# Kernel tuning notes

Measured on AMD Instinct MI355X. Metric: run time of the kernel, lower is better.

Reference implementation:

```python
import jax, jax.numpy as jnp
import numpy as np
from jax import lax

B, T, P, I, H = 1024, 100, 50, 96, 1024  # batch, seq_dim, pred_dim, input_dim, hidden_dim


def _gru_cell(x, h, Wih, Whh, bih, bhh):
    # PyTorch GRU gate math. Wih:[3H,in], Whh:[3H,H]
    gi = x @ Wih.T + bih
    gh = h @ Whh.T + bhh
    ir, iz, i_n = jnp.split(gi, 3, axis=-1)
    hr, hz, h_n = jnp.split(gh, 3, axis=-1)
    r = jax.nn.sigmoid(ir + hr)
    z = jax.nn.sigmoid(iz + hz)
    n = jnp.tanh(i_n + r * h_n)
    return (1.0 - z) * n + z * h


def setup_inputs() -> dict:
    key = jax.random.key(0)
    ks = jax.random.split(key, 24)
    s = 1.0 / np.sqrt(H)

    def rn(k, shape):
        return jax.random.normal(k, shape, jnp.float32) * s

    inp = {"x": jax.random.normal(ks[0], (B, T, I), jnp.float32)}
    # encoder nn.GRU: layer 0 input I, layer 1 input H
    inp["enc_Wih0"] = rn(ks[1], (3 * H, I)); inp["enc_Whh0"] = rn(ks[2], (3 * H, H))
    inp["enc_bih0"] = rn(ks[3], (3 * H,));   inp["enc_bhh0"] = rn(ks[4], (3 * H,))
    inp["enc_Wih1"] = rn(ks[5], (3 * H, H)); inp["enc_Whh1"] = rn(ks[6], (3 * H, H))
    inp["enc_bih1"] = rn(ks[7], (3 * H,));   inp["enc_bhh1"] = rn(ks[8], (3 * H,))
    # decoder GRUCells (hidden->hidden)
    inp["dec_Wih0"] = rn(ks[9], (3 * H, H)); inp["dec_Whh0"] = rn(ks[10], (3 * H, H))
    inp["dec_bih0"] = rn(ks[11], (3 * H,));  inp["dec_bhh0"] = rn(ks[12], (3 * H,))
    inp["dec_Wih1"] = rn(ks[13], (3 * H, H)); inp["dec_Whh1"] = rn(ks[14], (3 * H, H))
    inp["dec_bih1"] = rn(ks[15], (3 * H,));  inp["dec_bhh1"] = rn(ks[16], (3 * H,))
    # fc_in: I->H, fc_out: H->I
    inp["fc_in_w"] = rn(ks[17], (H, I)); inp["fc_in_b"] = rn(ks[18], (H,))
    inp["fc_out_w"] = rn(ks[19], (I, H)); inp["fc_out_b"] = rn(ks[20], (I,))
    return inp


def reference(x, enc_Wih0, enc_Whh0, enc_bih0, enc_bhh0,
              enc_Wih1, enc_Whh1, enc_bih1, enc_bhh1,
              dec_Wih0, dec_Whh0, dec_bih0, dec_bhh0,
              dec_Wih1, dec_Whh1, dec_bih1, dec_bhh1,
              fc_in_w, fc_in_b, fc_out_w, fc_out_b):
    b = x.shape[0]
    h0 = jnp.zeros((b, H), x.dtype)
    xs = jnp.transpose(x[:, :P, :], (1, 0, 2))  # [P, B, I]

    def enc0(h, xt):
        h2 = _gru_cell(xt, h, enc_Wih0, enc_Whh0, enc_bih0, enc_bhh0)
        return h2, h2

    h_enc0, seq0 = lax.scan(enc0, h0, xs)

    def enc1(h, xt):
        h2 = _gru_cell(xt, h, enc_Wih1, enc_Whh1, enc_bih1, enc_bhh1)
        return h2, h2

    h_enc1, _ = lax.scan(enc1, h0, seq0)

    def dec_step(carry, _):
        frame, hd0, hd1 = carry
        y = frame @ fc_in_w.T + fc_in_b
        hd0 = _gru_cell(y, hd0, dec_Wih0, dec_Whh0, dec_bih0, dec_bhh0)
        hd1 = _gru_cell(hd0, hd1, dec_Wih1, dec_Whh1, dec_bih1, dec_bhh1)
        frame = hd1 @ fc_out_w.T + fc_out_b + frame
        return (frame, hd0, hd1), frame

    init = (x[:, P - 1, :], h_enc0, h_enc1)
    _, outs = lax.scan(dec_step, init, None, length=T - P)  # [T-P, B, I]
    out = jnp.concatenate([x[:, :P, :], jnp.transpose(outs, (1, 0, 2))], axis=1)
    return out
```

## Files before the change

### kernel.cpp

```cpp
#include <hip/hip_runtime.h>
#include <hip/hip_bf16.h>
#include <stdint.h>

#define Bsz 1024
#define Tt  100
#define Pp  50
#define Ii  96
#define Hh  1024
#define H3  3072

typedef __bf16 bf16x8 __attribute__((ext_vector_type(8)));
typedef float f32x4 __attribute__((ext_vector_type(4)));
typedef __hip_bfloat16 bf16;

__device__ __forceinline__ void llds16(const void* g, void* l) {
    __builtin_amdgcn_global_load_lds(
        (const __attribute__((address_space(1))) void*)g,
        (__attribute__((address_space(3))) void*)l,
        16, 0, 0);
}

__device__ __forceinline__ f32x4 ldb4(const bf16* p) {
    ushort4 u = *(const ushort4*)p;
    union { unsigned int i; float f; } c;
    f32x4 r;
    c.i = (unsigned int)u.x << 16; r[0] = c.f;
    c.i = (unsigned int)u.y << 16; r[1] = c.f;
    c.i = (unsigned int)u.z << 16; r[2] = c.f;
    c.i = (unsigned int)u.w << 16; r[3] = c.f;
    return r;
}

__device__ __forceinline__ void swz_decomp(int& bx, int& by, int& bz) {
    int gx = gridDim.x, gy = gridDim.y, gz = gridDim.z;
    int flat = blockIdx.x + gx * (blockIdx.y + gy * blockIdx.z);
    int tot = gx * gy * gz;
    if (!(tot & 7)) {
        int q = tot >> 3;
        flat = (flat & 7) * q + (flat >> 3);
    }
    bx = flat % gx;
    int rest = flat / gx;
    by = rest % gy;
    bz = rest / gy;
}

__global__ void wdesc_k(unsigned long long* slot, const void* A, const void* W,
                        const void* b, void* C, int K, int lda) {
    if (threadIdx.x == 0) {
        slot[0] = (unsigned long long)A;
        slot[1] = (unsigned long long)W;
        slot[2] = (unsigned long long)b;
        slot[3] = (unsigned long long)C;
        slot[4] = (unsigned long long)K;
        slot[5] = (unsigned long long)lda;
    }
}

__global__ void __launch_bounds__(256)
gemm_tab(const unsigned long long* __restrict__ tab, int base, int ndesc,
         const bf16* __restrict__ extraA)
{
    __shared__ bf16 As[128 * 64];
    __shared__ bf16 Ws[128 * 64];
    int flat = blockIdx.x;
    const int tot = ndesc * 192;
    if (!(tot & 7)) {
        int q = tot >> 3;
        flat = (flat & 7) * q + (flat >> 3);
    }
    const int g = flat / 192;
    const int local = flat - g * 192;
    const unsigned long long* dp = tab + (size_t)(base + g) * 8;
    const bf16* A = (const bf16*)dp[0];
    const bf16* W = (const bf16*)dp[1];
    const float* bias = (const float*)dp[2];
    bf16* C = (bf16*)dp[3];
    const int K = (int)dp[4];
    const int lda = (int)dp[5];
    if (!A) A = extraA;

    const int tn = (local % 24) * 128;
    const int tm = (local / 24) * 128;

    const int tid = threadIdx.x;
    const int lane = tid & 63;
    const int wid = tid >> 6;
    const int wr = (wid >> 1) * 64;
    const int wc = (wid & 1) * 64;
    const int srow = tid >> 3;
    const int schk = ((tid & 7) ^ (srow & 7)) * 8;
    const int sdst = tid * 16;
    const int fr = lane & 15;
    const int hi = lane >> 4;

    f32x4 acc[4][4] = {};

    const bf16* ga = A + (size_t)(tm + srow) * lda + schk;
    const bf16* gw = W + (size_t)(tn + srow) * K + schk;
    char* lA = (char*)As + sdst;
    char* lW = (char*)Ws + sdst;
    const int nk = K >> 6;

    for (int kt = 0; kt < nk; ++kt) {
#pragma unroll
        for (int m = 0; m < 4; ++m) {
            llds16(ga + (size_t)(32 * m) * lda, lA + 32 * m * 128);
            llds16(gw + (size_t)(32 * m) * K,  lW + 32 * m * 128);
        }
        ga += 64; gw += 64;
        __syncthreads();

#pragma unroll
        for (int kk = 0; kk < 2; ++kk) {
            bf16x8 af[4], wf[4];
            const int chk = (((kk << 2) + hi) ^ (fr & 7)) * 8;
#pragma unroll
            for (int i = 0; i < 4; ++i) {
                af[i] = *(const bf16x8*)&As[(wr + i * 16 + fr) * 64 + chk];
                wf[i] = *(const bf16x8*)&Ws[(wc + i * 16 + fr) * 64 + chk];
            }
#pragma unroll
            for (int mi = 0; mi < 4; ++mi)
#pragma unroll
                for (int ni = 0; ni < 4; ++ni)
                    acc[mi][ni] = __builtin_amdgcn_mfma_f32_16x16x32_bf16(
                        af[mi], wf[ni], acc[mi][ni], 0, 0, 0);
        }
        __syncthreads();
    }

    const int fq = hi * 4;
#pragma unroll
    for (int mi = 0; mi < 4; ++mi)
#pragma unroll
        for (int ni = 0; ni < 4; ++ni) {
            const int col = tn + wc + ni * 16 + fr;
            const float bv = bias[col];
#pragma unroll
            for (int r = 0; r < 4; ++r) {
                const int row = tm + wr + mi * 16 + fq + r;
                C[(size_t)row * H3 + col] = __float2bfloat16(acc[mi][ni][r] + bv);
            }
        }
}

__global__ void __launch_bounds__(256)
fuse_fg_k(const float* __restrict__ gp,
          const float* __restrict__ fin,
          float* __restrict__ fout,
          float* __restrict__ out_t,
          const bf16* __restrict__ W,
          const float* __restrict__ bias,
          bf16* __restrict__ C)
{
    __shared__ bf16 Af[128 * 136];
    __shared__ bf16 Ws[128 * 64];
    int flat = blockIdx.x;
    { int q = 192 >> 3; flat = (flat & 7) * q + (flat >> 3); }
    const int tn = (flat % 24) * 128;
    const int tm = (flat / 24) * 128;
    const int tid = threadIdx.x;

#pragma unroll
    for (int i = 0; i < 12; ++i) {
        int v = i * 256 + tid;
        int row = v / 24;
        int c4 = (v % 24) * 4;
        size_t go = (size_t)(tm + row) * Ii + c4;
        f32x4 s = {};
#pragma unroll
        for (int p = 0; p < 8; ++p)
            s += *(const f32x4*)(gp + (size_t)p * (Bsz * Ii) + go);
        f32x4 fv = *(const f32x4*)(fin + go) + s;
        if (tn == 0) {
            *(f32x4*)(fout + go) = fv;
            *(f32x4*)(out_t + (size_t)(tm + row) * (Tt * Ii) + c4) = fv;
        }
        ushort4 up;
        unsigned short* us = &up.x;
#pragma unroll
        for (int e = 0; e < 4; ++e) {
            bf16 bv = __float2bfloat16(fv[e]);
            us[e] = *(unsigned short*)&bv;
        }
        *(ushort4*)&Af[row * 136 + c4] = up;
    }
#pragma unroll
    for (int i = 0; i < 4; ++i) {
        int v = i * 256 + tid;
        int row = v >> 3;
        int c4 = 96 + (v & 7) * 4;
        ushort4 z; z.x = 0; z.y = 0; z.z = 0; z.w = 0;
        *(ushort4*)&Af[row * 136 + c4] = z;
    }

    const int lane = tid & 63;
    const int wid = tid >> 6;
    const int wr = (wid >> 1) * 64;
    const int wc = (wid & 1) * 64;
    const int srow = tid >> 3;
    const int schk = ((tid & 7) ^ (srow & 7)) * 8;
    const int sdst = tid * 16;
    const int fr = lane & 15;
    const int hi = lane >> 4;

    f32x4 acc[4][4] = {};
    const bf16* gw = W + (size_t)(tn + srow) * 128 + schk;
    char* lW = (char*)Ws + sdst;

    for (int kt = 0; kt < 2; ++kt) {
#pragma unroll
        for (int m = 0; m < 4; ++m)
            llds16(gw + (size_t)(32 * m) * 128, lW + 32 * m * 128);
        gw += 64;
        __syncthreads();
#pragma unroll
        for (int kk = 0; kk < 2; ++kk) {
            bf16x8 af[4], wf[4];
            const int wchk = (((kk << 2) + hi) ^ (fr & 7)) * 8;
            const int achk = kt * 64 + ((kk << 2) + hi) * 8;
#pragma unroll
            for (int i = 0; i < 4; ++i) {
                af[i] = *(const bf16x8*)&Af[(wr + i * 16 + fr) * 136 + achk];
                wf[i] = *(const bf16x8*)&Ws[(wc + i * 16 + fr) * 64 + wchk];
            }
#pragma unroll
            for (int mi = 0; mi < 4; ++mi)
#pragma unroll
                for (int ni = 0; ni < 4; ++ni)
                    acc[mi][ni] = __builtin_amdgcn_mfma_f32_16x16x32_bf16(
                        af[mi], wf[ni], acc[mi][ni], 0, 0, 0);
        }
        __syncthreads();
    }

    const int fq = hi * 4;
#pragma unroll
    for (int mi = 0; mi < 4; ++mi)
#pragma unroll
        for (int ni = 0; ni < 4; ++ni) {
            const int col = tn + wc + ni * 16 + fr;
            const float bv = bias[col];
#pragma unroll
            for (int r = 0; r < 4; ++r) {
                const int row = tm + wr + mi * 16 + fq + r;
                C[(size_t)row * H3 + col] = __float2bfloat16(acc[mi][ni][r] + bv);
            }
        }
}

template <bool OUT_BF16>
__global__ void __launch_bounds__(256)
gemm64(const bf16* __restrict__ A, const bf16* __restrict__ W,
       const float* __restrict__ bias, void* __restrict__ Cout,
       int M, int Nreal, int Ktot, int Ks, int lda, int ldc)
{
    __shared__ bf16 As[64 * 32];
    __shared__ bf16 Ws[64 * 32];
    int bx, by, bz;
    swz_decomp(bx, by, bz);
    const int s = bz;
    const float* bs = (s == 0) ? bias : nullptr;
    const int tid = threadIdx.x;
    const int lane = tid & 63;
    const int wid = tid >> 6;
    const int wr = (wid >> 1) * 32;
    const int wc = (wid & 1) * 32;
    const int tm = by * 64;
    const int tn = bx * 64;
    const int srow = tid >> 2;
    const int skb = (tid & 3) * 8;
    const int k0 = s * Ks;

    f32x4 acc[2][2] = {};

    const bf16* ga = A + (size_t)(tm + srow) * lda + k0 + skb;
    const bf16* gw = W + (size_t)(tn + srow) * Ktot + k0 + skb;
    bf16* lA = &As[srow * 32 + skb];
    bf16* lW = &Ws[srow * 32 + skb];
    const int nk = Ks >> 5;

    for (int kt = 0; kt < nk; ++kt) {
        llds16(ga, lA);
        llds16(gw, lW);
        ga += 32; gw += 32;
        __syncthreads();
        const int fr = lane & 15;
        const int kg = (lane >> 4) * 8;
        bf16x8 af[2], wf[2];
#pragma unroll
        for (int i = 0; i < 2; ++i) {
            af[i] = *(const bf16x8*)&As[(wr + i * 16 + fr) * 32 + kg];
            wf[i] = *(const bf16x8*)&Ws[(wc + i * 16 + fr) * 32 + kg];
        }
#pragma unroll
        for (int mi = 0; mi < 2; ++mi)
#pragma unroll
            for (int ni = 0; ni < 2; ++ni)
                acc[mi][ni] = __builtin_amdgcn_mfma_f32_16x16x32_bf16(
                    af[mi], wf[ni], acc[mi][ni], 0, 0, 0);
        __syncthreads();
    }

    float* Cf = (float*)Cout + (size_t)s * M * ldc;
    const int fr = lane & 15;
    const int fq = (lane >> 4) * 4;
#pragma unroll
    for (int mi = 0; mi < 2; ++mi)
#pragma unroll
        for (int ni = 0; ni < 2; ++ni) {
            const int col = tn + wc + ni * 16 + fr;
            if (col < Nreal) {
                const float bv = bs ? bs[col] : 0.f;
#pragma unroll
                for (int r = 0; r < 4; ++r) {
                    const int row = tm + wr + mi * 16 + fq + r;
                    const float v = acc[mi][ni][r] + bv;
                    if constexpr (OUT_BF16)
                        ((bf16*)Cout)[(size_t)row * ldc + col] = __float2bfloat16(v);
                    else
                        Cf[(size_t)row * ldc + col] = v;
                }
            }
        }
}

__global__ void cvt_k(const float* __restrict__ s, bf16* __restrict__ d, int n) {
    int i = blockIdx.x * blockDim.x + threadIdx.x;
    if (i < n) d[i] = __float2bfloat16(s[i]);
}

__global__ void cvtpad_k(const float* __restrict__ s, bf16* __restrict__ d, int n) {
    int o = blockIdx.x * blockDim.x + threadIdx.x;
    if (o >= n * 128) return;
    int r = o >> 7, c = o & 127;
    d[o] = __float2bfloat16(c < Ii ? s[(size_t)r * Ii + c] : 0.f);
}

__global__ void tpose_k(const float* __restrict__ x, bf16* __restrict__ d) {
    int o = blockIdx.x * blockDim.x + threadIdx.x;
    if (o >= Tt * Bsz * 128) return;
    int i = o & 127;
    int b = (o >> 7) & (Bsz - 1);
    int t = o >> 17;
    d[o] = __float2bfloat16(i < Ii ? x[((size_t)b * Tt + t) * Ii + i] : 0.f);
}

__global__ void tposeFcin_k(const float* __restrict__ w, bf16* __restrict__ d) {
    int o = blockIdx.x * blockDim.x + threadIdx.x;
    if (o >= 128 * Hh) return;
    int r = o >> 10;
    int c = o & (Hh - 1);
    float v = (r < Ii) ? w[(size_t)c * Ii + r] : 0.f;
    d[o] = __float2bfloat16(v);
}

__global__ void __launch_bounds__(256)
bcomb_k(const float* __restrict__ W, const float* __restrict__ v,
        const float* __restrict__ b2, float* __restrict__ o) {
    __shared__ float red[256];
    int n = blockIdx.x;
    float s = 0.f;
    for (int k = threadIdx.x; k < Hh; k += 256)
        s += W[(size_t)n * Hh + k] * v[k];
    red[threadIdx.x] = s;
    __syncthreads();
    for (int w = 128; w > 0; w >>= 1) {
        if (threadIdx.x < w) red[threadIdx.x] += red[threadIdx.x + w];
        __syncthreads();
    }
    if (threadIdx.x == 0) o[n] = red[0] + b2[n];
}

__global__ void prefix_k(const float* __restrict__ x, float* __restrict__ out) {
    int idx = blockIdx.x * blockDim.x + threadIdx.x;
    if (idx >= Bsz * Pp * Ii) return;
    int b = idx / (Pp * Ii);
    int r = idx % (Pp * Ii);
    out[(size_t)b * Tt * Ii + r] = x[(size_t)b * Tt * Ii + r];
}

__global__ void finit_k(const float* __restrict__ x, float* __restrict__ fr,
                        bf16* __restrict__ frb) {
    int idx = blockIdx.x * blockDim.x + threadIdx.x;
    if (idx >= Bsz * Ii) return;
    int b = idx / Ii;
    int i = idx % Ii;
    float v = x[(size_t)b * Tt * Ii + (Pp - 1) * Ii + i];
    fr[idx] = v;
    frb[(size_t)b * 128 + i] = __float2bfloat16(v);
}

#define CELL_BODY(IDX, GI, GH, H, HB)                                        \
    {                                                                        \
        int b_ = (IDX) >> 8;                                                 \
        int j_ = ((IDX) & 255) << 2;                                         \
        size_t base_ = (size_t)b_ * H3 + j_;                                 \
        f32x4 ir = ldb4((GI) + base_);                                       \
        f32x4 iz = ldb4((GI) + base_ + Hh);                                  \
        f32x4 in = ldb4((GI) + base_ + 2 * Hh);                              \
        f32x4 hr = ldb4((GH) + base_);                                       \
        f32x4 hz = ldb4((GH) + base_ + Hh);                                  \
        f32x4 hn = ldb4((GH) + base_ + 2 * Hh);                              \
        size_t hoff_ = (size_t)b_ * Hh + j_;                                 \
        f32x4 hold = *(const f32x4*)((H) + hoff_);                           \
        f32x4 hv;                                                            \
        ushort4 up;                                                          \
        unsigned short* us = &up.x;                                          \
        _Pragma("unroll")                                                    \
        for (int e = 0; e < 4; ++e) {                                        \
            float r = 1.f / (1.f + __expf(-(ir[e] + hr[e])));                \
            float z = 1.f / (1.f + __expf(-(iz[e] + hz[e])));                \
            float n = tanhf(in[e] + r * hn[e]);                              \
            float v = (1.f - z) * n + z * hold[e];                           \
            hv[e] = v;                                                       \
            bf16 bv = __float2bfloat16(v);                                   \
            us[e] = *(unsigned short*)&bv;                                   \
        }                                                                    \
        *(f32x4*)((H) + hoff_) = hv;                                         \
        *(ushort4*)((unsigned short*)(HB) + hoff_) = up;                     \
    }

__global__ void __launch_bounds__(256)
gru_cell_k(const bf16* __restrict__ gi, const bf16* __restrict__ gh,
           float* __restrict__ h, bf16* __restrict__ hb) {
    int idx = blockIdx.x * 256 + threadIdx.x;
    CELL_BODY(idx, gi, gh, h, hb);
}

__global__ void __launch_bounds__(256)
gru_cell2_k(const bf16* __restrict__ giA, const bf16* __restrict__ ghA,
            float* __restrict__ hA, bf16* __restrict__ hbA,
            const bf16* __restrict__ giB, const bf16* __restrict__ ghB,
            float* __restrict__ hB, bf16* __restrict__ hbB) {
    int bid = blockIdx.x;
    const bf16* gi = giA;
    const bf16* gh = ghA;
    float* h = hA;
    bf16* hb = hbA;
    if (bid >= 1024) {
        gi = giB; gh = ghB; h = hB; hb = hbB;
        bid -= 1024;
    }
    int idx = bid * 256 + threadIdx.x;
    CELL_BODY(idx, gi, gh, h, hb);
}

extern "C" void kernel_launch(void* const* d_in, const int* in_sizes, int n_in,
                              void* d_out, int out_size, void* d_ws, size_t ws_size,
                              hipStream_t stream) {
    const float* x      = (const float*)d_in[0];
    const float* eWih0  = (const float*)d_in[1];
    const float* eWhh0  = (const float*)d_in[2];
    const float* ebih0  = (const float*)d_in[3];
    const float* ebhh0  = (const float*)d_in[4];
    const float* eWih1  = (const float*)d_in[5];
    const float* eWhh1  = (const float*)d_in[6];
    const float* ebih1  = (const float*)d_in[7];
    const float* ebhh1  = (const float*)d_in[8];
    const float* dWih0  = (const float*)d_in[9];
    const float* dWhh0  = (const float*)d_in[10];
    const float* dbih0  = (const float*)d_in[11];
    const float* dbhh0  = (const float*)d_in[12];
    const float* dWih1  = (const float*)d_in[13];
    const float* dWhh1  = (const float*)d_in[14];
    const float* dbih1  = (const float*)d_in[15];
    const float* dbhh1  = (const float*)d_in[16];
    const float* fcin_w = (const float*)d_in[17];
    const float* fcin_b = (const float*)d_in[18];
    const float* fcout_w= (const float*)d_in[19];
    const float* fcout_b= (const float*)d_in[20];
    float* out = (float*)d_out;

    char* base = (char*)d_ws;
    size_t off = 0;
    auto alloc = [&](size_t bytes) -> void* {
        void* r = base + off;
        off += (bytes + 255) & ~(size_t)255;
        return r;
    };
    bf16* wWih0e = (bf16*)alloc((size_t)H3 * 128 * 2);
    bf16* wWhh0e = (bf16*)alloc((size_t)H3 * Hh * 2);
    bf16* wWih1e = (bf16*)alloc((size_t)H3 * Hh * 2);
    bf16* wWhh1e = (bf16*)alloc((size_t)H3 * Hh * 2);
    bf16* wWhh0d = (bf16*)alloc((size_t)H3 * Hh * 2);
    bf16* wWih1d = (bf16*)alloc((size_t)H3 * Hh * 2);
    bf16* wWhh1d = (bf16*)alloc((size_t)H3 * Hh * 2);
    bf16* wWih0d = (bf16*)alloc((size_t)H3 * Hh * 2);
    bf16* fcinT  = (bf16*)alloc((size_t)128 * Hh * 2);
    bf16* wWcomb = (bf16*)alloc((size_t)H3 * 128 * 2);
    float* bcomb = (float*)alloc((size_t)H3 * 4);
    bf16* wfcout = (bf16*)alloc((size_t)128 * Hh * 2);
    float* zbias = (float*)alloc((size_t)128 * 4);
    bf16* xbT    = (bf16*)alloc((size_t)Tt * Bsz * 128 * 2);
    bf16* gi1_p  = (bf16*)alloc((size_t)Bsz * H3 * 2);
    bf16* gh1_p  = (bf16*)alloc((size_t)Bsz * H3 * 2);
    bf16* gh0_p  = (bf16*)alloc((size_t)Bsz * H3 * 2);
    bf16* gi0_p  = (bf16*)alloc((size_t)Bsz * H3 * 2);
    float* h0    = (float*)alloc((size_t)Bsz * Hh * 4);
    float* h1    = (float*)alloc((size_t)Bsz * Hh * 4);
    bf16* h0b    = (bf16*)alloc((size_t)Bsz * Hh * 2);
    bf16* h1b    = (bf16*)alloc((size_t)Bsz * Hh * 2);
    float* gfc   = (float*)alloc((size_t)8 * Bsz * Ii * 4);
    float* fbuf0 = (float*)alloc((size_t)Bsz * Ii * 4);
    float* fbuf1 = (float*)alloc((size_t)Bsz * Ii * 4);
    bf16* frameb = (bf16*)alloc((size_t)Bsz * 128 * 2);
    unsigned long long* tab = (unsigned long long*)alloc(8 * 8 * 8);
    if (off > ws_size) return;

    auto cvt = [&](const float* s, bf16* d, int n) {
        cvt_k<<<dim3((n + 255) / 256), dim3(256), 0, stream>>>(s, d, n);
    };
    cvtpad_k<<<dim3((H3 * 128 + 255) / 256), dim3(256), 0, stream>>>(eWih0, wWih0e, H3);
    cvt(eWhh0, wWhh0e, H3 * Hh);
    cvt(eWih1, wWih1e, H3 * Hh);
    cvt(eWhh1, wWhh1e, H3 * Hh);
    cvt(dWih0, wWih0d, H3 * Hh);
    cvt(dWhh0, wWhh0d, H3 * Hh);
    cvt(dWih1, wWih1d, H3 * Hh);
    cvt(dWhh1, wWhh1d, H3 * Hh);
    (void)hipMemsetAsync(wfcout, 0, (size_t)128 * Hh * 2, stream);
    (void)hipMemsetAsync(wWcomb, 0, (size_t)H3 * 128 * 2, stream);
    (void)hipMemsetAsync(zbias, 0, (size_t)128 * 4, stream);
    (void)hipMemsetAsync(frameb, 0, (size_t)Bsz * 128 * 2, stream);
    cvt(fcout_w, wfcout, Ii * Hh);
    tposeFcin_k<<<dim3((128 * Hh + 255) / 256), dim3(256), 0, stream>>>(fcin_w, fcinT);
    gemm64<true><<<dim3(2, 48, 1), dim3(256), 0, stream>>>(
        wWih0d, fcinT, zbias, (void*)wWcomb, H3, Ii, Hh, Hh, Hh, 128);
    bcomb_k<<<dim3(H3), dim3(256), 0, stream>>>(dWih0, fcin_b, dbih0, bcomb);

    tpose_k<<<dim3((Tt * Bsz * 128 + 255) / 256), dim3(256), 0, stream>>>(x, xbT);
    prefix_k<<<dim3((Bsz * Pp * Ii + 255) / 256), dim3(256), 0, stream>>>(x, out);
    finit_k<<<dim3((Bsz * Ii + 255) / 256), dim3(256), 0, stream>>>(x, fbuf0, frameb);
    (void)hipMemsetAsync(h0, 0, (size_t)Bsz * Hh * 4, stream);
    (void)hipMemsetAsync(h1, 0, (size_t)Bsz * Hh * 4, stream);
    (void)hipMemsetAsync(h0b, 0, (size_t)Bsz * Hh * 2, stream);
    (void)hipMemsetAsync(h1b, 0, (size_t)Bsz * Hh * 2, stream);

    wdesc_k<<<1, 64, 0, stream>>>(tab + 0 * 8, h0b, wWih1e, ebih1, gi1_p, Hh, Hh);
    wdesc_k<<<1, 64, 0, stream>>>(tab + 1 * 8, h1b, wWhh1e, ebhh1, gh1_p, Hh, Hh);
    wdesc_k<<<1, 64, 0, stream>>>(tab + 2 * 8, h0b, wWhh0e, ebhh0, gh0_p, Hh, Hh);
    wdesc_k<<<1, 64, 0, stream>>>(tab + 3 * 8, nullptr, wWih0e, ebih0, gi0_p, 128, 128);
    wdesc_k<<<1, 64, 0, stream>>>(tab + 4 * 8, h0b, wWih1d, dbih1, gi1_p, Hh, Hh);
    wdesc_k<<<1, 64, 0, stream>>>(tab + 5 * 8, h1b, wWhh1d, dbhh1, gh1_p, Hh, Hh);
    wdesc_k<<<1, 64, 0, stream>>>(tab + 6 * 8, h0b, wWhh0d, dbhh0, gh0_p, Hh, Hh);
    wdesc_k<<<1, 64, 0, stream>>>(tab + 7 * 8, frameb, wWcomb, bcomb, gi0_p, 128, 128);

    gemm_tab<<<dim3(384), dim3(256), 0, stream>>>(tab, 2, 2, xbT);
    gru_cell_k<<<dim3(1024), dim3(256), 0, stream>>>(gi0_p, gh0_p, h0, h0b);
    for (int i = 0; i < Pp; ++i) {
        if (i < Pp - 1) {
            gemm_tab<<<dim3(768), dim3(256), 0, stream>>>(
                tab, 0, 4, xbT + (size_t)(i + 1) * Bsz * 128);
            gru_cell2_k<<<dim3(2048), dim3(256), 0, stream>>>(
                gi1_p, gh1_p, h1, h1b, gi0_p, gh0_p, h0, h0b);
        } else {
            gemm_tab<<<dim3(384), dim3(256), 0, stream>>>(tab, 0, 2, xbT);
            gru_cell_k<<<dim3(1024), dim3(256), 0, stream>>>(gi1_p, gh1_p, h1, h1b);
        }
    }

    gemm_tab<<<dim3(384), dim3(256), 0, stream>>>(tab, 6, 2, xbT);
    gru_cell_k<<<dim3(1024), dim3(256), 0, stream>>>(gi0_p, gh0_p, h0, h0b);
    for (int t = 0; t < Tt - Pp; ++t) {
        const bool last = (t == Tt - Pp - 1);
        if (!last) {
            gemm_tab<<<dim3(576), dim3(256), 0, stream>>>(tab, 4, 3, xbT);
        } else {
            gemm_tab<<<dim3(384), dim3(256), 0, stream>>>(tab, 4, 2, xbT);
        }
        gru_cell_k<<<dim3(1024), dim3(256), 0, stream>>>(gi1_p, gh1_p, h1, h1b);
        gemm64<false><<<dim3(2, 16, 8), dim3(256), 0, stream>>>(
            h1b, wfcout, fcout_b, (void*)gfc, Bsz, Ii, Hh, Hh / 8, Hh, Ii);
        fuse_fg_k<<<dim3(192), dim3(256), 0, stream>>>(
            gfc, (t & 1) ? fbuf1 : fbuf0, (t & 1) ? fbuf0 : fbuf1,
            out + (size_t)(Pp + t) * Ii, wWcomb, bcomb, gi0_p);
        if (!last) {
            gru_cell_k<<<dim3(1024), dim3(256), 0, stream>>>(gi0_p, gh0_p, h0, h0b);
        }
    }
}
```

Baseline: 5.073 ms.

## Fuse decoder GRU cells into fc_out and gi0 GEMM kernels

In the decoder loop the layer-1 GRU cell is merged with the split-K fc_out GEMM (cellfc_k), and the gi0 GEMM is merged with the layer-0 GRU cell epilogue (megafuse_k). This cuts per-step launches from five to three and skips the round trips of gi0 and separate cell passes through global memory. Layer-1 hidden state is now double-buffered so cellfc_k's split-K blocks can read the old h1 while others write the new one. The fused kernels run on fewer blocks (256 and 128), which lowers parallelism. The last step now also runs the layer-0 cell update, which is wasted work.

```diff
diff --git a/kernel.cpp b/kernel.cpp
--- a/kernel.cpp
+++ b/kernel.cpp
@@ -29,6 +29,12 @@
     c.i = (unsigned int)u.z << 16; r[2] = c.f;
     c.i = (unsigned int)u.w << 16; r[3] = c.f;
     return r;
+}
+
+__device__ __forceinline__ float b2f(bf16 v) {
+    union { unsigned int i; float f; } c;
+    c.i = (unsigned int)(*(unsigned short*)&v) << 16;
+    return c.f;
 }
 
 __device__ __forceinline__ void swz_decomp(int& bx, int& by, int& bz) {
@@ -146,24 +152,130 @@
 }
 
 __global__ void __launch_bounds__(256)
-fuse_fg_k(const float* __restrict__ gp,
-          const float* __restrict__ fin,
-          float* __restrict__ fout,
-          float* __restrict__ out_t,
-          const bf16* __restrict__ W,
-          const float* __restrict__ bias,
-          bf16* __restrict__ C)
+cellfc_k(const bf16* __restrict__ gi, const bf16* __restrict__ gh,
+         const float* __restrict__ hin, float* __restrict__ hout,
+         bf16* __restrict__ hb,
+         const bf16* __restrict__ W,
+         const float* __restrict__ bias,
+         float* __restrict__ gfc)
 {
-    __shared__ bf16 Af[128 * 136];
+    __shared__ bf16 Af[64 * 136];
+    __shared__ bf16 Ws[64 * 32];
+    int flat = blockIdx.x;
+    { int q = 256 >> 3; flat = (flat & 7) * q + (flat >> 3); }
+    const int s = flat >> 5;
+    const int rest = flat & 31;
+    const int tm = (rest >> 1) * 64;
+    const int tn = (rest & 1) * 64;
+    const int k0 = s * 128;
+    const int tid = threadIdx.x;
+
+#pragma unroll
+    for (int i = 0; i < 8; ++i) {
+        int c = i * 256 + tid;
+        int row = c >> 5;
+        int c4 = (c & 31) * 4;
+        int b = tm + row;
+        int j = k0 + c4;
+        size_t gbase = (size_t)b * H3 + j;
+        f32x4 ir = ldb4(gi + gbase);
+        f32x4 iz = ldb4(gi + gbase + Hh);
+        f32x4 in = ldb4(gi + gbase + 2 * Hh);
+        f32x4 hr = ldb4(gh + gbase);
+        f32x4 hz = ldb4(gh + gbase + Hh);
+        f32x4 hn = ldb4(gh + gbase + 2 * Hh);
+        size_t ho = (size_t)b * Hh + j;
+        f32x4 hold = *(const f32x4*)(hin + ho);
+        f32x4 hv;
+        ushort4 up;
+        unsigned short* us = &up.x;
+#pragma unroll
+        for (int e = 0; e < 4; ++e) {
+            float r = 1.f / (1.f + __expf(-(ir[e] + hr[e])));
+            float z = 1.f / (1.f + __expf(-(iz[e] + hz[e])));
+            float n = tanhf(in[e] + r * hn[e]);
+            float v = (1.f - z) * n + z * hold[e];
+            hv[e] = v;
+            bf16 bv = __float2bfloat16(v);
+            us[e] = *(unsigned short*)&bv;
+        }
+        *(f32x4*)(hout + ho) = hv;
+        *(ushort4*)((unsigned short*)hb + ho) = up;
+        *(ushort4*)&Af[row * 136 + c4] = up;
+    }
+    __syncthreads();
+
+    const int lane = tid & 63;
+    const int wid = tid >> 6;
+    const int wr = (wid >> 1) * 32;
+    const int wc = (wid & 1) * 32;
+    const int srow = tid >> 2;
+    const int skb = (tid & 3) * 8;
+    const int fr = lane & 15;
+    const int kg = (lane >> 4) * 8;
+
+    f32x4 acc[2][2] = {};
+    const bf16* gw = W + (size_t)(tn + srow) * Hh + k0 + skb;
+    bf16* lW = &Ws[srow * 32 + skb];
+
+    for (int kt = 0; kt < 4; ++kt) {
+        llds16(gw, lW);
+        gw += 32;
+        __syncthreads();
+        bf16x8 af[2], wf[2];
+#pragma unroll
+        for (int i = 0; i < 2; ++i) {
+            af[i] = *(const bf16x8*)&Af[(wr + i * 16 + fr) * 136 + kt * 32 + kg];
+            wf[i] = *(const bf16x8*)&Ws[(wc + i * 16 + fr) * 32 + kg];
+        }
+#pragma unroll
+        for (int mi = 0; mi < 2; ++mi)
+#pragma unroll
+            for (int ni = 0; ni < 2; ++ni)
+                acc[mi][ni] = __builtin_amdgcn_mfma_f32_16x16x32_bf16(
+                    af[mi], wf[ni], acc[mi][ni], 0, 0, 0);
+        __syncthreads();
+    }
+
+    float* Cf = gfc + (size_t)s * (Bsz * Ii);
+    const int fq = (lane >> 4) * 4;
+#pragma unroll
+    for (int mi = 0; mi < 2; ++mi)
+#pragma unroll
+        for (int ni = 0; ni < 2; ++ni) {
+            const int col = tn + wc + ni * 16 + fr;
+            if (col < Ii) {
+                const float bv = (s == 0) ? bias[col] : 0.f;
+#pragma unroll
+                for (int r = 0; r < 4; ++r) {
+                    const int row = tm + wr + mi * 16 + fq + r;
+                    Cf[(size_t)row * Ii + col] = acc[mi][ni][r] + bv;
+                }
+            }
+        }
+}
+
+__global__ void __launch_bounds__(256)
+megafuse_k(const float* __restrict__ gp,
+           const float* __restrict__ fin,
+           float* __restrict__ fout,
+           float* __restrict__ out_t,
+           const bf16* __restrict__ W,
+           const float* __restrict__ bias,
+           const bf16* __restrict__ gh,
+           float* __restrict__ h,
+           bf16* __restrict__ hb)
+{
+    __shared__ bf16 Af[64 * 136];
     __shared__ bf16 Ws[128 * 64];
     int flat = blockIdx.x;
-    { int q = 192 >> 3; flat = (flat & 7) * q + (flat >> 3); }
-    const int tn = (flat % 24) * 128;
-    const int tm = (flat / 24) * 128;
+    { int q = 128 >> 3; flat = (flat & 7) * q + (flat >> 3); }
+    const int tm = (flat >> 3) * 64;
+    const int jt = flat & 7;
     const int tid = threadIdx.x;
 
 #pragma unroll
-    for (int i = 0; i < 12; ++i) {
+    for (int i = 0; i < 6; ++i) {
         int v = i * 256 + tid;
         int row = v / 24;
         int c4 = (v % 24) * 4;
@@ -173,7 +285,7 @@
         for (int p = 0; p < 8; ++p)
             s += *(const f32x4*)(gp + (size_t)p * (Bsz * Ii) + go);
         f32x4 fv = *(const f32x4*)(fin + go) + s;
-        if (tn == 0) {
+        if (jt == 0) {
             *(f32x4*)(fout + go) = fv;
             *(f32x4*)(out_t + (size_t)(tm + row) * (Tt * Ii) + c4) = fv;
         }
@@ -187,7 +299,7 @@
         *(ushort4*)&Af[row * 136 + c4] = up;
     }
 #pragma unroll
-    for (int i = 0; i < 4; ++i) {
+    for (int i = 0; i < 2; ++i) {
         int v = i * 256 + tid;
         int row = v >> 3;
         int c4 = 96 + (v & 7) * 4;
@@ -197,55 +309,74 @@
 
     const int lane = tid & 63;
     const int wid = tid >> 6;
-    const int wr = (wid >> 1) * 64;
+    const int wr = (wid >> 1) * 32;
     const int wc = (wid & 1) * 64;
     const int srow = tid >> 3;
     const int schk = ((tid & 7) ^ (srow & 7)) * 8;
     const int sdst = tid * 16;
     const int fr = lane & 15;
     const int hi = lane >> 4;
-
-    f32x4 acc[4][4] = {};
-    const bf16* gw = W + (size_t)(tn + srow) * 128 + schk;
     char* lW = (char*)Ws + sdst;
 
-    for (int kt = 0; kt < 2; ++kt) {
-#pragma unroll
-        for (int m = 0; m < 4; ++m)
-            llds16(gw + (size_t)(32 * m) * 128, lW + 32 * m * 128);
-        gw += 64;
-        __syncthreads();
-#pragma unroll
-        for (int kk = 0; kk < 2; ++kk) {
-            bf16x8 af[4], wf[4];
-            const int wchk = (((kk << 2) + hi) ^ (fr & 7)) * 8;
-            const int achk = kt * 64 + ((kk << 2) + hi) * 8;
-#pragma unroll
-            for (int i = 0; i < 4; ++i) {
-                af[i] = *(const bf16x8*)&Af[(wr + i * 16 + fr) * 136 + achk];
-                wf[i] = *(const bf16x8*)&Ws[(wc + i * 16 + fr) * 64 + wchk];
+    f32x4 acc[3][2][4] = {};
+#pragma unroll
+    for (int g = 0; g < 3; ++g) {
+        const bf16* gw = W + (size_t)(g * 1024 + jt * 128 + srow) * 128 + schk;
+        for (int kt = 0; kt < 2; ++kt) {
+            __syncthreads();
+#pragma unroll
+            for (int m = 0; m < 4; ++m)
+                llds16(gw + (size_t)(32 * m) * 128, lW + 32 * m * 128);
+            gw += 64;
+            __syncthreads();
+#pragma unroll
+            for (int kk = 0; kk < 2; ++kk) {
+                bf16x8 af[2], wf[4];
+                const int wchk = (((kk << 2) + hi) ^ (fr & 7)) * 8;
+                const int achk = kt * 64 + ((kk << 2) + hi) * 8;
+#pragma unroll
+                for (int i = 0; i < 2; ++i)
+                    af[i] = *(const bf16x8*)&Af[(wr + i * 16 + fr) * 136 + achk];
+#pragma unroll
+                for (int i = 0; i < 4; ++i)
+                    wf[i] = *(const bf16x8*)&Ws[(wc + i * 16 + fr) * 64 + wchk];
+#pragma unroll
+                for (int mi = 0; mi < 2; ++mi)
+#pragma unroll
+                    for (int ni = 0; ni < 4; ++ni)
+                        acc[g][mi][ni] = __builtin_amdgcn_mfma_f32_16x16x32_bf16(
+                            af[mi], wf[ni], acc[g][mi][ni], 0, 0, 0);
             }
-#pragma unroll
-            for (int mi = 0; mi < 4; ++mi)
-#pragma unroll
-                for (int ni = 0; ni < 4; ++ni)
-                    acc[mi][ni] = __builtin_amdgcn_mfma_f32_16x16x32_bf16(
-                        af[mi], wf[ni], acc[mi][ni], 0, 0, 0);
-        }
-        __syncthreads();
+        }
     }
 
     const int fq = hi * 4;
 #pragma unroll
-    for (int mi = 0; mi < 4; ++mi)
+    for (int mi = 0; mi < 2; ++mi)
 #pragma unroll
         for (int ni = 0; ni < 4; ++ni) {
-            const int col = tn + wc + ni * 16 + fr;
-            const float bv = bias[col];
+            const int j = jt * 128 + wc + ni * 16 + fr;
+            const float br = bias[j];
+            const float bz = bias[1024 + j];
+            const float bn = bias[2048 + j];
 #pragma unroll
             for (int r = 0; r < 4; ++r) {
                 const int row = tm + wr + mi * 16 + fq + r;
-                C[(size_t)row * H3 + col] = __float2bfloat16(acc[mi][ni][r] + bv);
+                const float ir = acc[0][mi][ni][r] + br;
+                const float iz = acc[1][mi][ni][r] + bz;
+                const float in_ = acc[2][mi][ni][r] + bn;
+                size_t gbase = (size_t)row * H3 + j;
+                const float hr = b2f(gh[gbase]);
+                const float hz = b2f(gh[gbase + Hh]);
+                const float hn = b2f(gh[gbase + 2 * Hh]);
+                size_t ho = (size_t)row * Hh + j;
+                const float hold = h[ho];
+                float rr = 1.f / (1.f + __expf(-(ir + hr)));
+                float zz = 1.f / (1.f + __expf(-(iz + hz)));
+                float nn = tanhf(in_ + rr * hn);
+                float v = (1.f - zz) * nn + zz * hold;
+                h[ho] = v;
+                hb[ho] = __float2bfloat16(v);
             }
         }
 }
@@ -499,7 +630,8 @@
     bf16* gh0_p  = (bf16*)alloc((size_t)Bsz * H3 * 2);
     bf16* gi0_p  = (bf16*)alloc((size_t)Bsz * H3 * 2);
     float* h0    = (float*)alloc((size_t)Bsz * Hh * 4);
-    float* h1    = (float*)alloc((size_t)Bsz * Hh * 4);
+    float* h1A   = (float*)alloc((size_t)Bsz * Hh * 4);
+    float* h1B   = (float*)alloc((size_t)Bsz * Hh * 4);
     bf16* h0b    = (bf16*)alloc((size_t)Bsz * Hh * 2);
     bf16* h1b    = (bf16*)alloc((size_t)Bsz * Hh * 2);
     float* gfc   = (float*)alloc((size_t)8 * Bsz * Ii * 4);
@@ -534,7 +666,7 @@
     prefix_k<<<dim3((Bsz * Pp * Ii + 255) / 256), dim3(256), 0, stream>>>(x, out);
     finit_k<<<dim3((Bsz * Ii + 255) / 256), dim3(256), 0, stream>>>(x, fbuf0, frameb);
     (void)hipMemsetAsync(h0, 0, (size_t)Bsz * Hh * 4, stream);
-    (void)hipMemsetAsync(h1, 0, (size_t)Bsz * Hh * 4, stream);
+    (void)hipMemsetAsync(h1A, 0, (size_t)Bsz * Hh * 4, stream);
     (void)hipMemsetAsync(h0b, 0, (size_t)Bsz * Hh * 2, stream);
     (void)hipMemsetAsync(h1b, 0, (size_t)Bsz * Hh * 2, stream);
 
@@ -554,10 +686,10 @@
             gemm_tab<<<dim3(768), dim3(256), 0, stream>>>(
                 tab, 0, 4, xbT + (size_t)(i + 1) * Bsz * 128);
             gru_cell2_k<<<dim3(2048), dim3(256), 0, stream>>>(
-                gi1_p, gh1_p, h1, h1b, gi0_p, gh0_p, h0, h0b);
+                gi1_p, gh1_p, h1A, h1b, gi0_p, gh0_p, h0, h0b);
         } else {
             gemm_tab<<<dim3(384), dim3(256), 0, stream>>>(tab, 0, 2, xbT);
-            gru_cell_k<<<dim3(1024), dim3(256), 0, stream>>>(gi1_p, gh1_p, h1, h1b);
+            gru_cell_k<<<dim3(1024), dim3(256), 0, stream>>>(gi1_p, gh1_p, h1A, h1b);
         }
     }
 
@@ -565,19 +697,15 @@
     gru_cell_k<<<dim3(1024), dim3(256), 0, stream>>>(gi0_p, gh0_p, h0, h0b);
     for (int t = 0; t < Tt - Pp; ++t) {
         const bool last = (t == Tt - Pp - 1);
-        if (!last) {
+        if (!last)
             gemm_tab<<<dim3(576), dim3(256), 0, stream>>>(tab, 4, 3, xbT);
-        } else {
+        else
             gemm_tab<<<dim3(384), dim3(256), 0, stream>>>(tab, 4, 2, xbT);
-        }
-        gru_cell_k<<<dim3(1024), dim3(256), 0, stream>>>(gi1_p, gh1_p, h1, h1b);
-        gemm64<false><<<dim3(2, 16, 8), dim3(256), 0, stream>>>(
-            h1b, wfcout, fcout_b, (void*)gfc, Bsz, Ii, Hh, Hh / 8, Hh, Ii);
-        fuse_fg_k<<<dim3(192), dim3(256), 0, stream>>>(
+        cellfc_k<<<dim3(256), dim3(256), 0, stream>>>(
+            gi1_p, gh1_p, (t & 1) ? h1B : h1A, (t & 1) ? h1A : h1B, h1b,
+            wfcout, fcout_b, gfc);
+        megafuse_k<<<dim3(128), dim3(256), 0, stream>>>(
             gfc, (t & 1) ? fbuf1 : fbuf0, (t & 1) ? fbuf0 : fbuf1,
-            out + (size_t)(Pp + t) * Ii, wWcomb, bcomb, gi0_p);
-        if (!last) {
-            gru_cell_k<<<dim3(1024), dim3(256), 0, stream>>>(gi0_p, gh0_p, h0, h0b);
-        }
-    }
-}
+            out + (size_t)(Pp + t) * Ii, wWcomb, bcomb, gh0_p, h0, h0b);
+    }
+}
```

Result: slower. 5.419 ms (+6.8%).
